# Optimization experiments

Hardware: AMD Instinct MI355X
Metric: run time of the kernel (lower is better)

## Reference

```python
import jax, jax.numpy as jnp
import numpy as np

EMBED = 256
HEADS = 8
HEAD_DIM = EMBED // HEADS
K = 7          # kernel_size
DIL = 1        # dilation
PAD = DIL * (K - 1) // 2  # 3
B, H, W = 4, 56, 56


def setup_inputs() -> dict:
    key = jax.random.key(0)
    ks = jax.random.split(key, 9)
    d = {"x": jax.random.normal(ks[0], (B, H, W, EMBED), jnp.float32)}
    for i, name in enumerate(["wq", "wk", "wv", "wo"]):
        d[name] = jax.random.normal(ks[1 + i], (EMBED, EMBED), jnp.float32) * 0.02
    for i, name in enumerate(["bq", "bk", "bv", "bo"]):
        d[name] = jax.random.normal(ks[5 + i], (EMBED,), jnp.float32) * 0.02
    return d


def _unfold(t):
    # t: [N, d, H, W] -> [N, d, K*K, H, W]; zero padding (matches F.unfold),
    # so out-of-bounds neighbors contribute logit 0, NOT -inf (faithful to source).
    h, w = t.shape[2], t.shape[3]
    tp = jnp.pad(t, ((0, 0), (0, 0), (PAD, PAD), (PAD, PAD)))
    patches = [tp[:, :, i * DIL:i * DIL + h, j * DIL:j * DIL + w]
               for i in range(K) for j in range(K)]  # fixed K*K=49 offsets
    return jnp.stack(patches, axis=2)


def reference(x, wq, bq, wk, bk, wv, bv, wo, bo):
    b, h, w, c = x.shape
    scale = HEAD_DIM ** -0.5
    q = x @ wq.T + bq
    k = x @ wk.T + bk
    v = x @ wv.T + bv

    def to_nh(t):  # [B,H,W,C] -> [B*heads, head_dim, H, W]
        return t.reshape(b, h, w, HEADS, HEAD_DIM).transpose(0, 3, 4, 1, 2).reshape(b * HEADS, HEAD_DIM, h, w)

    q, k, v = to_nh(q), to_nh(k), to_nh(v)
    k_unf = _unfold(k)  # [N, d, K2, H, W]
    v_unf = _unfold(v)
    logits = jnp.einsum('ndhw,ndkhw->nkhw', q, k_unf) * scale  # [N, K2, H, W]
    attn = jax.nn.softmax(logits, axis=1)
    out = jnp.einsum('nkhw,ndkhw->ndhw', attn, v_unf)  # [N, d, H, W]
    out = out.reshape(b, HEADS, HEAD_DIM, h, w).transpose(0, 3, 4, 1, 2).reshape(b, h, w, c)
    return out @ wo.T + bo
```

## Files before the change

kernel.cpp:

```cpp
#include <hip/hip_runtime.h>

typedef unsigned int u32;
typedef unsigned short u16;
typedef __attribute__((ext_vector_type(8))) short bf16x8;
typedef __attribute__((ext_vector_type(4))) float f32x4;

#define T_TOK 12544
#define EMB   256
#define IMG   56
#define SCALE 0.17677669529663689f
#define HALO  196
#define KSTR  40
#define VTSTR 224
#define PSTR  232

__device__ __forceinline__ u32 bf16_rtne(float f) {
    u32 u = __builtin_bit_cast(u32, f);
    return (u + 0x7fffu + ((u >> 16) & 1u)) >> 16;
}
__device__ __forceinline__ float bf16_to_f(u32 h) { return __builtin_bit_cast(float, h << 16); }

#define GLD16(g, l) __builtin_amdgcn_global_load_lds( \
    (const __attribute__((address_space(1))) u32*)(g), \
    (__attribute__((address_space(3))) u32*)(l), 16, 0, 0)

__global__ __launch_bounds__(256) void convert_kernel(
    const float* __restrict__ x, const float* __restrict__ wq, const float* __restrict__ wk,
    const float* __restrict__ wv, const float* __restrict__ wo,
    u16* __restrict__ xh, u16* __restrict__ bsh,
    u16* __restrict__ boh, u16* __restrict__ bol) {
    const int i = blockIdx.x * 256 + threadIdx.x;
    const int NX4 = T_TOK * EMB / 4;
    if (i < NX4) {
        const float4 f = ((const float4*)x)[i];
        const float vf[4] = {f.x, f.y, f.z, f.w};
        ushort4 hv;
        u16* hp = (u16*)&hv;
        #pragma unroll
        for (int c = 0; c < 4; ++c) hp[c] = (u16)bf16_rtne(vf[c]);
        ((ushort4*)xh)[i] = hv;
    } else {
        const int j = i - NX4;
        const int w = j >> 14, widx = j & 16383;
        const float* src = (w == 0) ? wq : (w == 1) ? wk : (w == 2) ? wv : wo;
        const float4 f = ((const float4*)src)[widx];
        const float vf[4] = {f.x, f.y, f.z, f.w};
        if (w < 3) {
            ushort4 hv;
            u16* hp = (u16*)&hv;
            #pragma unroll
            for (int c = 0; c < 4; ++c) hp[c] = (u16)bf16_rtne(vf[c]);
            ((ushort4*)bsh)[(w << 14) + widx] = hv;
        } else {
            ushort4 hv, lv;
            u16* hp = (u16*)&hv; u16* lp = (u16*)&lv;
            #pragma unroll
            for (int c = 0; c < 4; ++c) {
                const u32 h = bf16_rtne(vf[c]);
                hp[c] = (u16)h;
                lp[c] = (u16)bf16_rtne(vf[c] - bf16_to_f(h));
            }
            ((ushort4*)boh)[widx] = hv;
            ((ushort4*)bol)[widx] = lv;
        }
    }
}

__global__ __launch_bounds__(256) void qkv_mfma(
    const u16* __restrict__ xh, const u16* __restrict__ bsh,
    const float* __restrict__ bq, const float* __restrict__ bk, const float* __restrict__ bv,
    u16* __restrict__ qb, u16* __restrict__ kb, u16* __restrict__ vb) {
    __shared__ __attribute__((aligned(16))) u16 sA[128 * 32];
    __shared__ __attribute__((aligned(16))) u16 sB[128 * 32];
    const int nBase = blockIdx.x * 128;
    const int mBase = blockIdx.y * 128;
    const int tid = threadIdx.x, wv = tid >> 6, ln = tid & 63;
    const int lrow = ln & 15, lqd = ln >> 4;
    const int wm = (wv & 1) * 64, wn = (wv >> 1) * 64;
    const int c0 = wv * 128 + ln, r0 = c0 >> 2, kc0 = c0 & 3;
    const int c1 = c0 + 64,       r1 = c1 >> 2, kc1 = c1 & 3;
    const size_t gA0 = (size_t)(mBase + r0) * EMB + kc0 * 8;
    const size_t gA1 = (size_t)(mBase + r1) * EMB + kc1 * 8;
    const size_t gB0 = (size_t)(nBase + r0) * EMB + kc0 * 8;
    const size_t gB1 = (size_t)(nBase + r1) * EMB + kc1 * 8;
    const int l0 = (wv * 128) * 8, l1 = (wv * 128 + 64) * 8;

    f32x4 acc[4][4];
    #pragma unroll
    for (int mi = 0; mi < 4; ++mi)
        #pragma unroll
        for (int ni = 0; ni < 4; ++ni)
            acc[mi][ni] = (f32x4){0.f, 0.f, 0.f, 0.f};

    for (int kt = 0; kt < 8; ++kt) {
        const int k0 = kt * 32;
        GLD16(xh  + gA0 + k0, sA + l0);
        GLD16(xh  + gA1 + k0, sA + l1);
        GLD16(bsh + gB0 + k0, sB + l0);
        GLD16(bsh + gB1 + k0, sB + l1);
        __syncthreads();
        bf16x8 af[4], bf[4];
        #pragma unroll
        for (int mi = 0; mi < 4; ++mi)
            af[mi] = *(const bf16x8*)&sA[(wm + mi * 16 + lrow) * 32 + lqd * 8];
        #pragma unroll
        for (int ni = 0; ni < 4; ++ni)
            bf[ni] = *(const bf16x8*)&sB[(wn + ni * 16 + lrow) * 32 + lqd * 8];
        #pragma unroll
        for (int mi = 0; mi < 4; ++mi)
            #pragma unroll
            for (int ni = 0; ni < 4; ++ni)
                acc[mi][ni] = __builtin_amdgcn_mfma_f32_16x16x32_bf16(af[mi], bf[ni], acc[mi][ni], 0, 0, 0);
        __syncthreads();
    }

    const int which = nBase >> 8;
    const float* bias = (which == 0) ? bq : (which == 1) ? bk : bv;
    u16* dst = (which == 0) ? qb : (which == 1) ? kb : vb;
    #pragma unroll
    for (int ni = 0; ni < 4; ++ni) {
        const int ncol = nBase + wn + ni * 16 + lrow;
        const int c = ncol & 255;
        const float bz = bias[c];
        #pragma unroll
        for (int mi = 0; mi < 4; ++mi) {
            #pragma unroll
            for (int r = 0; r < 4; ++r) {
                const int row = mBase + wm + mi * 16 + lqd * 4 + r;
                dst[(size_t)row * EMB + c] = (u16)bf16_rtne(acc[mi][ni][r] + bz);
            }
        }
    }
}

__global__ __launch_bounds__(256) void out_mfma(
    const u16* __restrict__ aoh, const u16* __restrict__ aol,
    const u16* __restrict__ boh, const u16* __restrict__ bol,
    const float* __restrict__ bo, float* __restrict__ out) {
    __shared__ __attribute__((aligned(16))) u16 sAh[64 * 32];
    __shared__ __attribute__((aligned(16))) u16 sAl[64 * 32];
    __shared__ __attribute__((aligned(16))) u16 sBh[128 * 32];
    __shared__ __attribute__((aligned(16))) u16 sBl[128 * 32];
    const int nBase = blockIdx.x * 128;
    const int mBase = blockIdx.y * 64;
    const int tid = threadIdx.x, wv = tid >> 6, ln = tid & 63;
    const int lrow = ln & 15, lqd = ln >> 4;
    const int cA = wv * 64 + ln, rA = cA >> 2, kcA = cA & 3;
    const size_t gA = (size_t)(mBase + rA) * EMB + kcA * 8;
    const int lA = (wv * 64) * 8;
    const int c0 = wv * 128 + ln, r0 = c0 >> 2, kc0 = c0 & 3;
    const int c1 = c0 + 64,       r1 = c1 >> 2, kc1 = c1 & 3;
    const size_t gB0 = (size_t)(nBase + r0) * EMB + kc0 * 8;
    const size_t gB1 = (size_t)(nBase + r1) * EMB + kc1 * 8;
    const int l0 = (wv * 128) * 8, l1 = (wv * 128 + 64) * 8;

    f32x4 acc[4][2];
    #pragma unroll
    for (int mi = 0; mi < 4; ++mi)
        #pragma unroll
        for (int ni = 0; ni < 2; ++ni)
            acc[mi][ni] = (f32x4){0.f, 0.f, 0.f, 0.f};

    for (int kt = 0; kt < 8; ++kt) {
        const int k0 = kt * 32;
        GLD16(aoh + gA + k0, sAh + lA);
        GLD16(aol + gA + k0, sAl + lA);
        GLD16(boh + gB0 + k0, sBh + l0);
        GLD16(boh + gB1 + k0, sBh + l1);
        GLD16(bol + gB0 + k0, sBl + l0);
        GLD16(bol + gB1 + k0, sBl + l1);
        __syncthreads();
        bf16x8 ah[4], al[4], bh[2], bl[2];
        #pragma unroll
        for (int mi = 0; mi < 4; ++mi) {
            ah[mi] = *(const bf16x8*)&sAh[(mi * 16 + lrow) * 32 + lqd * 8];
            al[mi] = *(const bf16x8*)&sAl[(mi * 16 + lrow) * 32 + lqd * 8];
        }
        #pragma unroll
        for (int ni = 0; ni < 2; ++ni) {
            bh[ni] = *(const bf16x8*)&sBh[(wv * 32 + ni * 16 + lrow) * 32 + lqd * 8];
            bl[ni] = *(const bf16x8*)&sBl[(wv * 32 + ni * 16 + lrow) * 32 + lqd * 8];
        }
        #pragma unroll
        for (int mi = 0; mi < 4; ++mi)
            #pragma unroll
            for (int ni = 0; ni < 2; ++ni) {
                acc[mi][ni] = __builtin_amdgcn_mfma_f32_16x16x32_bf16(ah[mi], bh[ni], acc[mi][ni], 0, 0, 0);
                acc[mi][ni] = __builtin_amdgcn_mfma_f32_16x16x32_bf16(al[mi], bh[ni], acc[mi][ni], 0, 0, 0);
                acc[mi][ni] = __builtin_amdgcn_mfma_f32_16x16x32_bf16(ah[mi], bl[ni], acc[mi][ni], 0, 0, 0);
            }
        __syncthreads();
    }

    #pragma unroll
    for (int ni = 0; ni < 2; ++ni) {
        const int ncol = nBase + wv * 32 + ni * 16 + lrow;
        const float bz = bo[ncol];
        #pragma unroll
        for (int mi = 0; mi < 4; ++mi) {
            #pragma unroll
            for (int r = 0; r < 4; ++r) {
                const int row = mBase + mi * 16 + lqd * 4 + r;
                out[(size_t)row * EMB + ncol] = acc[mi][ni][r] + bz;
            }
        }
    }
}

__global__ __launch_bounds__(256, 2) void attn_kernel(
    const u16* __restrict__ qb, const u16* __restrict__ kb, const u16* __restrict__ vb,
    u16* __restrict__ aoh, u16* __restrict__ aol) {
    __shared__ __attribute__((aligned(16))) u16 smem[30976];
    u16* sK  = smem;
    u16* sVT = smem + 8960;
    u16* sP  = smem + 16128;
    u16* sV1 = sP;

    const int tid = threadIdx.x;
    const int w = tid >> 6, ln = tid & 63;
    const int lrow = ln & 15, lqd = ln >> 4;
    const int img = blockIdx.z >> 3, head = blockIdx.z & 7;
    const int ty0 = blockIdx.y * 8, tx0 = blockIdx.x * 8;

    for (int i = tid; i < 1792; i += 256) {
        const int mv = (i >= 896) ? 1 : 0;
        const int ii = i - 896 * mv;
        const int p = ii >> 2, c = ii & 3;
        const int pyh = p / 14, pxh = p - pyh * 14;
        const int gy = ty0 - 3 + pyh, gx = tx0 - 3 + pxh;
        u16* dst = (mv ? sV1 : sK) + p * KSTR + c * 8;
        if (p < HALO && (unsigned)gy < 56u && (unsigned)gx < 56u) {
            const size_t tt = ((size_t)img * IMG + gy) * IMG + gx;
            *(uint4*)dst = *(const uint4*)((mv ? vb : kb) + tt * EMB + head * 32 + c * 8);
        } else {
            *(uint4*)dst = (uint4){0u, 0u, 0u, 0u};
        }
    }
    __syncthreads();

    for (int i = tid; i < 896; i += 256) {
        const int d = i & 31, ho = i >> 5;
        u32 pk[4];
        #pragma unroll
        for (int j = 0; j < 4; ++j) {
            const u32 a = sV1[(ho * 8 + 2 * j)     * KSTR + d];
            const u32 b = sV1[(ho * 8 + 2 * j + 1) * KSTR + d];
            pk[j] = a | (b << 16);
        }
        *(uint4*)&sVT[d * VTSTR + ho * 8] = *(uint4*)pk;
    }

    const int mpix = w * 16 + lrow;
    const int qpy = mpix >> 3, qpx = mpix & 7;
    const size_t qtok = ((size_t)img * IMG + ty0 + qpy) * IMG + tx0 + qpx;
    const bf16x8 aq = *(const bf16x8*)&qb[qtok * EMB + head * 32 + lqd * 8];

    f32x4 ct[13];
    #pragma unroll
    for (int t = 0; t < 13; ++t) ct[t] = (f32x4){0.f, 0.f, 0.f, 0.f};
    #pragma unroll
    for (int t = 0; t < 13; ++t) {
        const bf16x8 bk = *(const bf16x8*)&sK[(t * 16 + lrow) * KSTR + lqd * 8];
        ct[t] = __builtin_amdgcn_mfma_f32_16x16x32_bf16(aq, bk, ct[t], 0, 0, 0);
    }

    int pys[4], pxs[4];
    #pragma unroll
    for (int r = 0; r < 4; ++r) {
        const int row = lqd * 4 + r;
        pys[r] = 2 * w + (row >> 3);
        pxs[r] = row & 7;
    }
    float mr4[4] = {-1e30f, -1e30f, -1e30f, -1e30f};
    #pragma unroll
    for (int t = 0; t < 13; ++t) {
        const int col = t * 16 + lrow;
        const int hy = col / 14, hx = col - 14 * hy;
        const bool okc = (col < HALO);
        #pragma unroll
        for (int r = 0; r < 4; ++r) {
            const bool ok = ((unsigned)(hy - pys[r]) < 7u) &
                            ((unsigned)(hx - pxs[r]) < 7u) & okc;
            const float lv = ok ? ct[t][r] * SCALE : -1e30f;
            ct[t][r] = lv;
            mr4[r] = fmaxf(mr4[r], lv);
        }
    }
    #pragma unroll
    for (int r = 0; r < 4; ++r) {
        float m = mr4[r];
        m = fmaxf(m, __shfl_xor(m, 1));
        m = fmaxf(m, __shfl_xor(m, 2));
        m = fmaxf(m, __shfl_xor(m, 4));
        m = fmaxf(m, __shfl_xor(m, 8));
        mr4[r] = m;
    }
    float sr4[4] = {0.f, 0.f, 0.f, 0.f};
    #pragma unroll
    for (int t = 0; t < 13; ++t)
        #pragma unroll
        for (int r = 0; r < 4; ++r) {
            const float e = __expf(ct[t][r] - mr4[r]);
            ct[t][r] = e;
            sr4[r] += e;
        }
    #pragma unroll
    for (int r = 0; r < 4; ++r) {
        float s = sr4[r];
        s += __shfl_xor(s, 1);
        s += __shfl_xor(s, 2);
        s += __shfl_xor(s, 4);
        s += __shfl_xor(s, 8);
        sr4[r] = 1.0f / s;
    }

    __syncthreads();

    u16* sPw = sP + w * 16 * PSTR;
    #pragma unroll
    for (int t = 0; t < 13; ++t)
        #pragma unroll
        for (int r = 0; r < 4; ++r)
            sPw[(lqd * 4 + r) * PSTR + t * 16 + lrow] = (u16)bf16_rtne(ct[t][r]);
    #pragma unroll
    for (int z = 0; z < 4; ++z) {
        const int idx = z * 64 + ln;
        sPw[(idx >> 4) * PSTR + 208 + (idx & 15)] = 0;
    }

    f32x4 o0 = (f32x4){0.f, 0.f, 0.f, 0.f};
    f32x4 o1 = (f32x4){0.f, 0.f, 0.f, 0.f};
    #pragma unroll
    for (int ks = 0; ks < 7; ++ks) {
        const bf16x8 ap  = *(const bf16x8*)&sPw[lrow * PSTR + ks * 32 + lqd * 8];
        const bf16x8 bv0 = *(const bf16x8*)&sVT[lrow * VTSTR + ks * 32 + lqd * 8];
        const bf16x8 bv1 = *(const bf16x8*)&sVT[(16 + lrow) * VTSTR + ks * 32 + lqd * 8];
        o0 = __builtin_amdgcn_mfma_f32_16x16x32_bf16(ap, bv0, o0, 0, 0, 0);
        o1 = __builtin_amdgcn_mfma_f32_16x16x32_bf16(ap, bv1, o1, 0, 0, 0);
    }

    #pragma unroll
    for (int r = 0; r < 4; ++r) {
        const int row = lqd * 4 + r;
        const int opy = 2 * w + (row >> 3), opx = row & 7;
        const size_t ot = ((size_t)img * IMG + ty0 + opy) * IMG + tx0 + opx;
        const float inv = sr4[r];
        const float v0 = o0[r] * inv;
        const float v1 = o1[r] * inv;
        const size_t base = ot * EMB + head * 32;
        const u32 h0 = bf16_rtne(v0);
        aoh[base + lrow] = (u16)h0;
        aol[base + lrow] = (u16)bf16_rtne(v0 - bf16_to_f(h0));
        const u32 h1 = bf16_rtne(v1);
        aoh[base + 16 + lrow] = (u16)h1;
        aol[base + 16 + lrow] = (u16)bf16_rtne(v1 - bf16_to_f(h1));
    }
}

extern "C" void kernel_launch(void* const* d_in, const int* in_sizes, int n_in,
                              void* d_out, int out_size, void* d_ws, size_t ws_size,
                              hipStream_t stream) {
    const float* x  = (const float*)d_in[0];
    const float* wq = (const float*)d_in[1];
    const float* wk = (const float*)d_in[2];
    const float* wv = (const float*)d_in[3];
    const float* wo = (const float*)d_in[4];
    const float* bq = (const float*)d_in[5];
    const float* bk = (const float*)d_in[6];
    const float* bv = (const float*)d_in[7];
    const float* bo = (const float*)d_in[8];
    float* out = (float*)d_out;

    char* ws = (char*)d_ws;
    u16* xh  = (u16*)(ws);
    u16* qb  = (u16*)(ws +  6422528);
    u16* kb  = (u16*)(ws + 12845056);
    u16* vb  = (u16*)(ws + 19267584);
    u16* aoh = (u16*)(ws + 25690112);
    u16* aol = (u16*)(ws + 32112640);
    u16* bsh = (u16*)(ws + 38535168);
    u16* boh = (u16*)(ws + 38928384);
    u16* bol = (u16*)(ws + 39059456);

    convert_kernel<<<3392, 256, 0, stream>>>(x, wq, wk, wv, wo, xh, bsh, boh, bol);
    qkv_mfma<<<dim3(6, 98), 256, 0, stream>>>(xh, bsh, bq, bk, bv, qb, kb, vb);
    attn_kernel<<<dim3(7, 7, 32), 256, 0, stream>>>(qb, kb, vb, aoh, aol);
    out_mfma<<<dim3(2, 196), 256, 0, stream>>>(aoh, aol, boh, bol, bo, out);
}
```

Baseline: 136.4 us.

## Fuse x bf16 conversion into QKV GEMM, retile output GEMM, shrink attention LDS

```diff
diff --git a/kernel.cpp b/kernel.cpp
--- a/kernel.cpp
+++ b/kernel.cpp
@@ -19,55 +19,45 @@
     return (u + 0x7fffu + ((u >> 16) & 1u)) >> 16;
 }
 __device__ __forceinline__ float bf16_to_f(u32 h) { return __builtin_bit_cast(float, h << 16); }
+__device__ __forceinline__ u32 pk2(float a, float b) {
+    return bf16_rtne(a) | (bf16_rtne(b) << 16);
+}
 
 #define GLD16(g, l) __builtin_amdgcn_global_load_lds( \
     (const __attribute__((address_space(1))) u32*)(g), \
     (__attribute__((address_space(3))) u32*)(l), 16, 0, 0)
 
-__global__ __launch_bounds__(256) void convert_kernel(
-    const float* __restrict__ x, const float* __restrict__ wq, const float* __restrict__ wk,
+__global__ __launch_bounds__(256) void weight_convert(
+    const float* __restrict__ wq, const float* __restrict__ wk,
     const float* __restrict__ wv, const float* __restrict__ wo,
-    u16* __restrict__ xh, u16* __restrict__ bsh,
-    u16* __restrict__ boh, u16* __restrict__ bol) {
+    u16* __restrict__ bsh, u16* __restrict__ boh, u16* __restrict__ bol) {
     const int i = blockIdx.x * 256 + threadIdx.x;
-    const int NX4 = T_TOK * EMB / 4;
-    if (i < NX4) {
-        const float4 f = ((const float4*)x)[i];
-        const float vf[4] = {f.x, f.y, f.z, f.w};
+    const int w = i >> 14, widx = i & 16383;
+    const float* src = (w == 0) ? wq : (w == 1) ? wk : (w == 2) ? wv : wo;
+    const float4 f = ((const float4*)src)[widx];
+    const float vf[4] = {f.x, f.y, f.z, f.w};
+    if (w < 3) {
         ushort4 hv;
         u16* hp = (u16*)&hv;
         #pragma unroll
         for (int c = 0; c < 4; ++c) hp[c] = (u16)bf16_rtne(vf[c]);
-        ((ushort4*)xh)[i] = hv;
+        ((ushort4*)bsh)[(w << 14) + widx] = hv;
     } else {
-        const int j = i - NX4;
-        const int w = j >> 14, widx = j & 16383;
-        const float* src = (w == 0) ? wq : (w == 1) ? wk : (w == 2) ? wv : wo;
-        const float4 f = ((const float4*)src)[widx];
-        const float vf[4] = {f.x, f.y, f.z, f.w};
-        if (w < 3) {
-            ushort4 hv;
-            u16* hp = (u16*)&hv;
-            #pragma unroll
-            for (int c = 0; c < 4; ++c) hp[c] = (u16)bf16_rtne(vf[c]);
-            ((ushort4*)bsh)[(w << 14) + widx] = hv;
-        } else {
-            ushort4 hv, lv;
-            u16* hp = (u16*)&hv; u16* lp = (u16*)&lv;
-            #pragma unroll
-            for (int c = 0; c < 4; ++c) {
-                const u32 h = bf16_rtne(vf[c]);
-                hp[c] = (u16)h;
-                lp[c] = (u16)bf16_rtne(vf[c] - bf16_to_f(h));
-            }
-            ((ushort4*)boh)[widx] = hv;
-            ((ushort4*)bol)[widx] = lv;
-        }
+        ushort4 hv, lv;
+        u16* hp = (u16*)&hv; u16* lp = (u16*)&lv;
+        #pragma unroll
+        for (int c = 0; c < 4; ++c) {
+            const u32 h = bf16_rtne(vf[c]);
+            hp[c] = (u16)h;
+            lp[c] = (u16)bf16_rtne(vf[c] - bf16_to_f(h));
+        }
+        ((ushort4*)boh)[widx] = hv;
+        ((ushort4*)bol)[widx] = lv;
     }
 }
 
 __global__ __launch_bounds__(256) void qkv_mfma(
-    const u16* __restrict__ xh, const u16* __restrict__ bsh,
+    const float* __restrict__ x, const u16* __restrict__ bsh,
     const float* __restrict__ bq, const float* __restrict__ bk, const float* __restrict__ bv,
     u16* __restrict__ qb, u16* __restrict__ kb, u16* __restrict__ vb) {
     __shared__ __attribute__((aligned(16))) u16 sA[128 * 32];
@@ -94,10 +84,22 @@
 
     for (int kt = 0; kt < 8; ++kt) {
         const int k0 = kt * 32;
-        GLD16(xh  + gA0 + k0, sA + l0);
-        GLD16(xh  + gA1 + k0, sA + l1);
         GLD16(bsh + gB0 + k0, sB + l0);
         GLD16(bsh + gB1 + k0, sB + l1);
+        {
+            const float4 f0 = *(const float4*)&x[gA0 + k0];
+            const float4 f1 = *(const float4*)&x[gA0 + k0 + 4];
+            const uint4 p = {pk2(f0.x, f0.y), pk2(f0.z, f0.w),
+                             pk2(f1.x, f1.y), pk2(f1.z, f1.w)};
+            *(uint4*)&sA[c0 * 8] = p;
+        }
+        {
+            const float4 f0 = *(const float4*)&x[gA1 + k0];
+            const float4 f1 = *(const float4*)&x[gA1 + k0 + 4];
+            const uint4 p = {pk2(f0.x, f0.y), pk2(f0.z, f0.w),
+                             pk2(f1.x, f1.y), pk2(f1.z, f1.w)};
+            *(uint4*)&sA[c1 * 8] = p;
+        }
         __syncthreads();
         bf16x8 af[4], bf[4];
         #pragma unroll
@@ -139,82 +141,65 @@
     const float* __restrict__ bo, float* __restrict__ out) {
     __shared__ __attribute__((aligned(16))) u16 sAh[64 * 32];
     __shared__ __attribute__((aligned(16))) u16 sAl[64 * 32];
-    __shared__ __attribute__((aligned(16))) u16 sBh[128 * 32];
-    __shared__ __attribute__((aligned(16))) u16 sBl[128 * 32];
-    const int nBase = blockIdx.x * 128;
+    __shared__ __attribute__((aligned(16))) u16 sBh[64 * 32];
+    __shared__ __attribute__((aligned(16))) u16 sBl[64 * 32];
+    const int nBase = blockIdx.x * 64;
     const int mBase = blockIdx.y * 64;
     const int tid = threadIdx.x, wv = tid >> 6, ln = tid & 63;
     const int lrow = ln & 15, lqd = ln >> 4;
-    const int cA = wv * 64 + ln, rA = cA >> 2, kcA = cA & 3;
+    const int rA = tid >> 2, kcA = tid & 3;
     const size_t gA = (size_t)(mBase + rA) * EMB + kcA * 8;
-    const int lA = (wv * 64) * 8;
-    const int c0 = wv * 128 + ln, r0 = c0 >> 2, kc0 = c0 & 3;
-    const int c1 = c0 + 64,       r1 = c1 >> 2, kc1 = c1 & 3;
-    const size_t gB0 = (size_t)(nBase + r0) * EMB + kc0 * 8;
-    const size_t gB1 = (size_t)(nBase + r1) * EMB + kc1 * 8;
-    const int l0 = (wv * 128) * 8, l1 = (wv * 128 + 64) * 8;
-
-    f32x4 acc[4][2];
-    #pragma unroll
-    for (int mi = 0; mi < 4; ++mi)
-        #pragma unroll
-        for (int ni = 0; ni < 2; ++ni)
-            acc[mi][ni] = (f32x4){0.f, 0.f, 0.f, 0.f};
+    const size_t gB = (size_t)(nBase + rA) * EMB + kcA * 8;
+    const int lA = wv * 64 * 8;
+
+    f32x4 acc[4];
+    #pragma unroll
+    for (int mi = 0; mi < 4; ++mi) acc[mi] = (f32x4){0.f, 0.f, 0.f, 0.f};
 
     for (int kt = 0; kt < 8; ++kt) {
         const int k0 = kt * 32;
         GLD16(aoh + gA + k0, sAh + lA);
         GLD16(aol + gA + k0, sAl + lA);
-        GLD16(boh + gB0 + k0, sBh + l0);
-        GLD16(boh + gB1 + k0, sBh + l1);
-        GLD16(bol + gB0 + k0, sBl + l0);
-        GLD16(bol + gB1 + k0, sBl + l1);
+        GLD16(boh + gB + k0, sBh + lA);
+        GLD16(bol + gB + k0, sBl + lA);
         __syncthreads();
-        bf16x8 ah[4], al[4], bh[2], bl[2];
+        bf16x8 ah[4], al[4];
         #pragma unroll
         for (int mi = 0; mi < 4; ++mi) {
             ah[mi] = *(const bf16x8*)&sAh[(mi * 16 + lrow) * 32 + lqd * 8];
             al[mi] = *(const bf16x8*)&sAl[(mi * 16 + lrow) * 32 + lqd * 8];
         }
-        #pragma unroll
-        for (int ni = 0; ni < 2; ++ni) {
-            bh[ni] = *(const bf16x8*)&sBh[(wv * 32 + ni * 16 + lrow) * 32 + lqd * 8];
-            bl[ni] = *(const bf16x8*)&sBl[(wv * 32 + ni * 16 + lrow) * 32 + lqd * 8];
-        }
-        #pragma unroll
-        for (int mi = 0; mi < 4; ++mi)
-            #pragma unroll
-            for (int ni = 0; ni < 2; ++ni) {
-                acc[mi][ni] = __builtin_amdgcn_mfma_f32_16x16x32_bf16(ah[mi], bh[ni], acc[mi][ni], 0, 0, 0);
-                acc[mi][ni] = __builtin_amdgcn_mfma_f32_16x16x32_bf16(al[mi], bh[ni], acc[mi][ni], 0, 0, 0);
-                acc[mi][ni] = __builtin_amdgcn_mfma_f32_16x16x32_bf16(ah[mi], bl[ni], acc[mi][ni], 0, 0, 0);
-            }
+        const bf16x8 bh = *(const bf16x8*)&sBh[(wv * 16 + lrow) * 32 + lqd * 8];
+        const bf16x8 bl = *(const bf16x8*)&sBl[(wv * 16 + lrow) * 32 + lqd * 8];
+        #pragma unroll
+        for (int mi = 0; mi < 4; ++mi) {
+            acc[mi] = __builtin_amdgcn_mfma_f32_16x16x32_bf16(ah[mi], bh, acc[mi], 0, 0, 0);
+            acc[mi] = __builtin_amdgcn_mfma_f32_16x16x32_bf16(al[mi], bh, acc[mi], 0, 0, 0);
+            acc[mi] = __builtin_amdgcn_mfma_f32_16x16x32_bf16(ah[mi], bl, acc[mi], 0, 0, 0);
+        }
         __syncthreads();
     }
 
-    #pragma unroll
-    for (int ni = 0; ni < 2; ++ni) {
-        const int ncol = nBase + wv * 32 + ni * 16 + lrow;
-        const float bz = bo[ncol];
-        #pragma unroll
-        for (int mi = 0; mi < 4; ++mi) {
-            #pragma unroll
-            for (int r = 0; r < 4; ++r) {
-                const int row = mBase + mi * 16 + lqd * 4 + r;
-                out[(size_t)row * EMB + ncol] = acc[mi][ni][r] + bz;
-            }
-        }
-    }
-}
-
-__global__ __launch_bounds__(256, 2) void attn_kernel(
+    const int ncol = nBase + wv * 16 + lrow;
+    const float bz = bo[ncol];
+    #pragma unroll
+    for (int mi = 0; mi < 4; ++mi) {
+        #pragma unroll
+        for (int r = 0; r < 4; ++r) {
+            const int row = mBase + mi * 16 + lqd * 4 + r;
+            out[(size_t)row * EMB + ncol] = acc[mi][r] + bz;
+        }
+    }
+}
+
+__global__ __launch_bounds__(256, 3) void attn_kernel(
     const u16* __restrict__ qb, const u16* __restrict__ kb, const u16* __restrict__ vb,
     u16* __restrict__ aoh, u16* __restrict__ aol) {
-    __shared__ __attribute__((aligned(16))) u16 smem[30976];
+    __shared__ __attribute__((aligned(16))) u16 smem[25088];
     u16* sK  = smem;
-    u16* sVT = smem + 8960;
-    u16* sP  = smem + 16128;
-    u16* sV1 = sP;
+    u16* sV1 = smem + 8960;
+    u16* sVT = smem + 17920;
+    u16* sP  = smem;
 
     const int tid = threadIdx.x;
     const int w = tid >> 6, ln = tid & 63;
@@ -372,18 +357,17 @@
     float* out = (float*)d_out;
 
     char* ws = (char*)d_ws;
-    u16* xh  = (u16*)(ws);
-    u16* qb  = (u16*)(ws +  6422528);
-    u16* kb  = (u16*)(ws + 12845056);
-    u16* vb  = (u16*)(ws + 19267584);
-    u16* aoh = (u16*)(ws + 25690112);
-    u16* aol = (u16*)(ws + 32112640);
-    u16* bsh = (u16*)(ws + 38535168);
-    u16* boh = (u16*)(ws + 38928384);
-    u16* bol = (u16*)(ws + 39059456);
-
-    convert_kernel<<<3392, 256, 0, stream>>>(x, wq, wk, wv, wo, xh, bsh, boh, bol);
-    qkv_mfma<<<dim3(6, 98), 256, 0, stream>>>(xh, bsh, bq, bk, bv, qb, kb, vb);
+    u16* qb  = (u16*)(ws);
+    u16* kb  = (u16*)(ws +  6422528);
+    u16* vb  = (u16*)(ws + 12845056);
+    u16* aoh = (u16*)(ws + 19267584);
+    u16* aol = (u16*)(ws + 25690112);
+    u16* bsh = (u16*)(ws + 32112640);
+    u16* boh = (u16*)(ws + 32505856);
+    u16* bol = (u16*)(ws + 32636928);
+
+    weight_convert<<<256, 256, 0, stream>>>(wq, wk, wv, wo, bsh, boh, bol);
+    qkv_mfma<<<dim3(6, 98), 256, 0, stream>>>(x, bsh, bq, bk, bv, qb, kb, vb);
     attn_kernel<<<dim3(7, 7, 32), 256, 0, stream>>>(qb, kb, vb, aoh, aol);
-    out_mfma<<<dim3(2, 196), 256, 0, stream>>>(aoh, aol, boh, bol, bo, out);
-}
+    out_mfma<<<dim3(4, 196), 256, 0, stream>>>(aoh, aol, boh, bol, bo, out);
+}
```

New measurement: 133.8 us. No clear change (-1.9%).
